# Optimization experiments

Measured on AMD Instinct MI355X. Metric: run time of the kernel, lower is better.

Reference implementation:

```python
import jax, jax.numpy as jnp
import numpy as np

TEMPERATURE = 0.07
EPS = 1e-12  # matches torch F.normalize eps
B, D = 16384, 128


def setup_inputs() -> dict:
    key = jax.random.key(0)
    k1, k2 = jax.random.split(key)
    anchor = jax.random.normal(k1, (B, D), dtype=jnp.float32)
    positive = jax.random.normal(k2, (B, D), dtype=jnp.float32)
    return {"anchor": anchor, "positive": positive}


def _l2_normalize(x):
    # torch F.normalize: x / max(||x||, eps)
    n = jnp.sqrt(jnp.sum(x * x, axis=-1, keepdims=True))
    return x / jnp.maximum(n, EPS)


def reference(anchor, positive):
    a = _l2_normalize(anchor)          # [B, D]
    p = _l2_normalize(positive)        # [B, D]
    pos_sim = jnp.sum(a * p, axis=-1) / TEMPERATURE            # [B]
    sim = jnp.matmul(a, p.T) / TEMPERATURE                     # [B, B]
    neg_inf = jnp.finfo(sim.dtype).min
    bsz = sim.shape[0]
    eye = jnp.eye(bsz, dtype=bool)
    neg_sim = jnp.where(eye, neg_inf, sim)                     # diag masked
    logits = jnp.concatenate([pos_sim[:, None], neg_sim], axis=1)  # [B, B+1]
    # cross-entropy with label 0: -log_softmax(logits)[:, 0]
    lse = jax.nn.logsumexp(logits, axis=1)
    loss = lse - logits[:, 0]
    return jnp.mean(loss)
```

## Files before the change

kernel.cpp:

```cpp
#include <hip/hip_runtime.h>
#include <stdint.h>

#define NROWS 16384
#define DIM 128

typedef __attribute__((ext_vector_type(8))) __bf16 bf16x8;
typedef __attribute__((ext_vector_type(4))) float f32x4;
typedef __attribute__((ext_vector_type(4))) unsigned int u32x4;

constexpr float TEMP_INV = 1.0f / 0.07f;
constexpr float LOG2E = 1.4426950408889634f;
constexpr float LN2 = 0.69314718055994531f;
constexpr float KAPPA = LOG2E * TEMP_INV;
constexpr float SQRT_KAPPA = 4.53981600f;

__device__ __forceinline__ ushort f2bf(float x) {
  uint32_t u = __builtin_bit_cast(uint32_t, x);
  uint32_t r = (u + 0x7fffu + ((u >> 16) & 1u)) >> 16;
  return (ushort)r;
}

__global__ __launch_bounds__(256) void prep_kernel(
    const float* __restrict__ anchor, const float* __restrict__ positive,
    ushort* __restrict__ abar, ushort* __restrict__ pbar,
    float* __restrict__ pos_u)
{
  const int tid = threadIdx.x;
  const int row = blockIdx.x * 16 + (tid >> 4);
  const int c0 = (tid & 15) * 8;

  const float4* a4 = reinterpret_cast<const float4*>(anchor + (size_t)row * DIM + c0);
  const float4* p4 = reinterpret_cast<const float4*>(positive + (size_t)row * DIM + c0);
  float4 a0 = a4[0], a1 = a4[1];
  float4 p0 = p4[0], p1 = p4[1];

  float af[8] = {a0.x, a0.y, a0.z, a0.w, a1.x, a1.y, a1.z, a1.w};
  float pf[8] = {p0.x, p0.y, p0.z, p0.w, p1.x, p1.y, p1.z, p1.w};

  float sa = 0.f, sp = 0.f, dp = 0.f;
#pragma unroll
  for (int j = 0; j < 8; ++j) {
    sa += af[j] * af[j];
    sp += pf[j] * pf[j];
    dp += af[j] * pf[j];
  }
#pragma unroll
  for (int m = 1; m <= 8; m <<= 1) {
    sa += __shfl_xor(sa, m, 64);
    sp += __shfl_xor(sp, m, 64);
    dp += __shfl_xor(dp, m, 64);
  }
  float inva = 1.0f / fmaxf(sqrtf(sa), 1e-12f);
  float invp = 1.0f / fmaxf(sqrtf(sp), 1e-12f);
  float ca = inva * SQRT_KAPPA;
  float cp = invp * SQRT_KAPPA;

  ushort ua[8], up[8];
#pragma unroll
  for (int j = 0; j < 8; ++j) {
    ua[j] = f2bf(af[j] * ca);
    up[j] = f2bf(pf[j] * cp);
  }
  *reinterpret_cast<uint4*>(abar + (size_t)row * DIM + c0) = *reinterpret_cast<uint4*>(ua);
  *reinterpret_cast<uint4*>(pbar + (size_t)row * DIM + c0) = *reinterpret_cast<uint4*>(up);

  if ((tid & 15) == 0)
    pos_u[row] = dp * inva * invp * KAPPA;
}

#define NSPLIT 8
#define BM 512
#define CPB (NROWS / NSPLIT)
#define BN 32
#define NIT (CPB / BN)

__global__ __launch_bounds__(512, 2) void lse_kernel(
    const ushort* __restrict__ abar,
    const ushort* __restrict__ pbar,
    float* __restrict__ sbuf )
{
  __shared__ alignas(16) char lds[2][BN * 256];

  const int tid = threadIdx.x;
  const int l = tid & 63;
  const int w = tid >> 6;
  const int r15 = l & 15;
  const int hi = l >> 4;

  const int bid = blockIdx.x;
  const int csplit = bid & 7;
  const int rowblk = bid >> 3;
  const int row0 = rowblk * BM + w * 64;
  const int col0 = csplit * CPB;

  const char* abase = (const char*)abar;
  const char* pbase = (const char*)pbar;

  bf16x8 afrag[4][4];
#pragma unroll
  for (int rg = 0; rg < 4; ++rg)
#pragma unroll
    for (int kk = 0; kk < 4; ++kk) {
      size_t off = (size_t)(row0 + rg * 16 + r15) * 256 + (size_t)(kk * 32 + hi * 8) * 2;
      u32x4 v = *reinterpret_cast<const u32x4*>(abase + off);
      afrag[rg][kk] = __builtin_bit_cast(bf16x8, v);
    }

  float s[4][4];
#pragma unroll
  for (int rg = 0; rg < 4; ++rg)
#pragma unroll
    for (int rr = 0; rr < 4; ++rr) s[rg][rr] = 0.f;

  const int strow = tid >> 4;
  const int stlds = strow * 256 + (((tid & 15) * 16) ^ ((strow & 7) << 4));

  u32x4 stg = *reinterpret_cast<const u32x4*>(pbase + (size_t)col0 * 256 + tid * 16);
  *reinterpret_cast<u32x4*>(&lds[0][stlds]) = stg;
  __syncthreads();

  for (int it = 0; it < NIT; ++it) {
    const int cur = it & 1;
    if (it + 1 < NIT)
      stg = *reinterpret_cast<const u32x4*>(
          pbase + (size_t)(col0 + (it + 1) * BN) * 256 + tid * 16);

#pragma unroll
    for (int ct = 0; ct < 2; ++ct) {
      const int tr = ct * 16 + r15;
      const int sw = (tr & 7) << 4;
      const char* base = &lds[cur][tr * 256];
      bf16x8 bfrag[4];
#pragma unroll
      for (int kk = 0; kk < 4; ++kk) {
        const int cb = kk * 64 + hi * 16;
        u32x4 v = *reinterpret_cast<const u32x4*>(base + (cb ^ sw));
        bfrag[kk] = __builtin_bit_cast(bf16x8, v);
      }
#pragma unroll
      for (int rg = 0; rg < 4; ++rg) {
        f32x4 acc = {0.f, 0.f, 0.f, 0.f};
#pragma unroll
        for (int kk = 0; kk < 4; ++kk)
          acc = __builtin_amdgcn_mfma_f32_16x16x32_bf16(afrag[rg][kk], bfrag[kk], acc, 0, 0, 0);
        s[rg][0] += __builtin_amdgcn_exp2f(acc[0]);
        s[rg][1] += __builtin_amdgcn_exp2f(acc[1]);
        s[rg][2] += __builtin_amdgcn_exp2f(acc[2]);
        s[rg][3] += __builtin_amdgcn_exp2f(acc[3]);
      }
    }
    __syncthreads();
    if (it + 1 < NIT) {
      *reinterpret_cast<u32x4*>(&lds[cur ^ 1][stlds]) = stg;
      __syncthreads();
    }
  }

#pragma unroll
  for (int rg = 0; rg < 4; ++rg)
#pragma unroll
    for (int rr = 0; rr < 4; ++rr) {
      float v = s[rg][rr];
      v += __shfl_xor(v, 1, 64);
      v += __shfl_xor(v, 2, 64);
      v += __shfl_xor(v, 4, 64);
      v += __shfl_xor(v, 8, 64);
      if (r15 == 0) {
        int grow = row0 + rg * 16 + hi * 4 + rr;
        sbuf[(size_t)csplit * NROWS + grow] = v;
      }
    }
}

__global__ __launch_bounds__(512) void finalize_kernel(
    const float* __restrict__ sbuf, const float* __restrict__ pos_u,
    float* __restrict__ out)
{
  const int tid = threadIdx.x;
  float acc = 0.f;
  for (int r = tid; r < NROWS; r += 512) {
    float s = 0.f;
#pragma unroll
    for (int c = 0; c < NSPLIT; ++c) s += sbuf[(size_t)c * NROWS + r];
    acc += LN2 * (__builtin_amdgcn_logf(s) - pos_u[r]);
  }
#pragma unroll
  for (int m = 1; m <= 32; m <<= 1) acc += __shfl_xor(acc, m, 64);
  __shared__ float red[8];
  if ((tid & 63) == 0) red[tid >> 6] = acc;
  __syncthreads();
  if (tid < 8) {
    float v = red[tid];
    v += __shfl_xor(v, 1, 64);
    v += __shfl_xor(v, 2, 64);
    v += __shfl_xor(v, 4, 64);
    if (tid == 0) out[0] = v * (1.0f / (float)NROWS);
  }
}

extern "C" void kernel_launch(void* const* d_in, const int* in_sizes, int n_in,
                              void* d_out, int out_size, void* d_ws, size_t ws_size,
                              hipStream_t stream) {
  const float* anchor = (const float*)d_in[0];
  const float* positive = (const float*)d_in[1];
  char* ws = (char*)d_ws;

  ushort* abar = (ushort*)ws;
  ushort* pbar = (ushort*)(ws + (size_t)NROWS * DIM * 2);
  float* pos_u = (float*)(ws + (size_t)NROWS * DIM * 4);
  float* sbuf = (float*)(ws + (size_t)NROWS * DIM * 4 + (size_t)NROWS * 4);
  float* out = (float*)d_out;

  prep_kernel<<<NROWS / 16, 256, 0, stream>>>(anchor, positive, abar, pbar, pos_u);
  lse_kernel<<<NSPLIT * (NROWS / BM), 512, 0, stream>>>(abar, pbar, sbuf);
  finalize_kernel<<<1, 512, 0, stream>>>(sbuf, pos_u, out);
}
```

Before: 92.73 us.

## Use direct global-to-LDS async loads with 4-deep buffering and smaller row tiles

Replaces the register-staged double buffer for positive tiles with global_load_lds direct copies into a 4-slot LDS ring, prefetching two tiles ahead and using vmcnt waits plus a single barrier per iteration. Halves rows per block (BM 512→256) to raise occupancy to 4 blocks per CU, adds setprio around the MFMA/exp section, and splits the single-block finalize into a parallel per-block partial reduction plus a tiny second pass. The aim is to hide load latency and remove the extra sync, at the cost of halving the reuse of each loaded B tile, so each block does less compute per load.

```diff
diff --git a/kernel.cpp b/kernel.cpp
--- a/kernel.cpp
+++ b/kernel.cpp
@@ -20,6 +20,12 @@
   return (ushort)r;
 }
 
+__device__ __forceinline__ void gload_lds16(const void* g, void* l) {
+  __builtin_amdgcn_global_load_lds(
+      (const __attribute__((address_space(1))) unsigned int*)g,
+      (__attribute__((address_space(3))) unsigned int*)l, 16, 0, 0);
+}
+
 __global__ __launch_bounds__(256) void prep_kernel(
     const float* __restrict__ anchor, const float* __restrict__ positive,
     ushort* __restrict__ abar, ushort* __restrict__ pbar,
@@ -69,17 +75,18 @@
 }
 
 #define NSPLIT 8
-#define BM 512
+#define BM 256
 #define CPB (NROWS / NSPLIT)
 #define BN 32
 #define NIT (CPB / BN)
-
-__global__ __launch_bounds__(512, 2) void lse_kernel(
+#define NBUF 4
+
+__global__ __launch_bounds__(512, 4) void lse_kernel(
     const ushort* __restrict__ abar,
     const ushort* __restrict__ pbar,
     float* __restrict__ sbuf )
 {
-  __shared__ alignas(16) char lds[2][BN * 256];
+  __shared__ alignas(16) char lds[NBUF][BN * 256];
 
   const int tid = threadIdx.x;
   const int l = tid & 63;
@@ -90,15 +97,15 @@
   const int bid = blockIdx.x;
   const int csplit = bid & 7;
   const int rowblk = bid >> 3;
-  const int row0 = rowblk * BM + w * 64;
+  const int row0 = rowblk * BM + w * 32;
   const int col0 = csplit * CPB;
 
   const char* abase = (const char*)abar;
   const char* pbase = (const char*)pbar;
 
-  bf16x8 afrag[4][4];
-#pragma unroll
-  for (int rg = 0; rg < 4; ++rg)
+  bf16x8 afrag[2][4];
+#pragma unroll
+  for (int rg = 0; rg < 2; ++rg)
 #pragma unroll
     for (int kk = 0; kk < 4; ++kk) {
       size_t off = (size_t)(row0 + rg * 16 + r15) * 256 + (size_t)(kk * 32 + hi * 8) * 2;
@@ -106,30 +113,42 @@
       afrag[rg][kk] = __builtin_bit_cast(bf16x8, v);
     }
 
-  float s[4][4];
-#pragma unroll
-  for (int rg = 0; rg < 4; ++rg)
+  float s[2][4];
+#pragma unroll
+  for (int rg = 0; rg < 2; ++rg)
 #pragma unroll
     for (int rr = 0; rr < 4; ++rr) s[rg][rr] = 0.f;
 
-  const int strow = tid >> 4;
-  const int stlds = strow * 256 + (((tid & 15) * 16) ^ ((strow & 7) << 4));
-
-  u32x4 stg = *reinterpret_cast<const u32x4*>(pbase + (size_t)col0 * 256 + tid * 16);
-  *reinterpret_cast<u32x4*>(&lds[0][stlds]) = stg;
-  __syncthreads();
+  const int trow = w * 4 + (l >> 4);
+  const size_t src0 = (size_t)(col0 + trow) * 256 + (size_t)(((l & 15) ^ (trow & 7)) * 16);
+  void* ldst[NBUF];
+#pragma unroll
+  for (int b = 0; b < NBUF; ++b) ldst[b] = &lds[b][w * 1024];
+
+  gload_lds16(pbase + src0, ldst[0]);
+  __builtin_amdgcn_sched_barrier(0);
+  gload_lds16(pbase + src0 + 8192, ldst[1]);
+  __builtin_amdgcn_sched_barrier(0);
 
   for (int it = 0; it < NIT; ++it) {
-    const int cur = it & 1;
-    if (it + 1 < NIT)
-      stg = *reinterpret_cast<const u32x4*>(
-          pbase + (size_t)(col0 + (it + 1) * BN) * 256 + tid * 16);
-
+    if (it < NIT - 1) {
+      asm volatile("s_waitcnt vmcnt(1)" ::: "memory");
+    } else {
+      asm volatile("s_waitcnt vmcnt(0)" ::: "memory");
+    }
+    __builtin_amdgcn_s_barrier();
+    asm volatile("" ::: "memory");
+    __builtin_amdgcn_sched_barrier(0);
+
+    if (it + 2 < NIT)
+      gload_lds16(pbase + src0 + (size_t)(it + 2) * 8192, ldst[(it + 2) & 3]);
+
+    const char* bufp = lds[it & 3];
 #pragma unroll
     for (int ct = 0; ct < 2; ++ct) {
       const int tr = ct * 16 + r15;
       const int sw = (tr & 7) << 4;
-      const char* base = &lds[cur][tr * 256];
+      const char* base = bufp + tr * 256;
       bf16x8 bfrag[4];
 #pragma unroll
       for (int kk = 0; kk < 4; ++kk) {
@@ -137,8 +156,9 @@
         u32x4 v = *reinterpret_cast<const u32x4*>(base + (cb ^ sw));
         bfrag[kk] = __builtin_bit_cast(bf16x8, v);
       }
-#pragma unroll
-      for (int rg = 0; rg < 4; ++rg) {
+      __builtin_amdgcn_s_setprio(1);
+#pragma unroll
+      for (int rg = 0; rg < 2; ++rg) {
         f32x4 acc = {0.f, 0.f, 0.f, 0.f};
 #pragma unroll
         for (int kk = 0; kk < 4; ++kk)
@@ -148,16 +168,12 @@
         s[rg][2] += __builtin_amdgcn_exp2f(acc[2]);
         s[rg][3] += __builtin_amdgcn_exp2f(acc[3]);
       }
-    }
-    __syncthreads();
-    if (it + 1 < NIT) {
-      *reinterpret_cast<u32x4*>(&lds[cur ^ 1][stlds]) = stg;
-      __syncthreads();
-    }
-  }
-
-#pragma unroll
-  for (int rg = 0; rg < 4; ++rg)
+      __builtin_amdgcn_s_setprio(0);
+    }
+  }
+
+#pragma unroll
+  for (int rg = 0; rg < 2; ++rg)
 #pragma unroll
     for (int rr = 0; rr < 4; ++rr) {
       float v = s[rg][rr];
@@ -172,30 +188,31 @@
     }
 }
 
-__global__ __launch_bounds__(512) void finalize_kernel(
+__global__ __launch_bounds__(256) void finalize1(
     const float* __restrict__ sbuf, const float* __restrict__ pos_u,
-    float* __restrict__ out)
+    float* __restrict__ partial)
 {
   const int tid = threadIdx.x;
-  float acc = 0.f;
-  for (int r = tid; r < NROWS; r += 512) {
-    float s = 0.f;
-#pragma unroll
-    for (int c = 0; c < NSPLIT; ++c) s += sbuf[(size_t)c * NROWS + r];
-    acc += LN2 * (__builtin_amdgcn_logf(s) - pos_u[r]);
-  }
+  const int r = blockIdx.x * 256 + tid;
+  float ssum = 0.f;
+#pragma unroll
+  for (int c = 0; c < NSPLIT; ++c) ssum += sbuf[(size_t)c * NROWS + r];
+  float acc = LN2 * (__builtin_amdgcn_logf(ssum) - pos_u[r]);
 #pragma unroll
   for (int m = 1; m <= 32; m <<= 1) acc += __shfl_xor(acc, m, 64);
-  __shared__ float red[8];
+  __shared__ float red[4];
   if ((tid & 63) == 0) red[tid >> 6] = acc;
   __syncthreads();
-  if (tid < 8) {
-    float v = red[tid];
-    v += __shfl_xor(v, 1, 64);
-    v += __shfl_xor(v, 2, 64);
-    v += __shfl_xor(v, 4, 64);
-    if (tid == 0) out[0] = v * (1.0f / (float)NROWS);
-  }
+  if (tid == 0) partial[blockIdx.x] = red[0] + red[1] + red[2] + red[3];
+}
+
+__global__ __launch_bounds__(64) void finalize2(
+    const float* __restrict__ partial, float* __restrict__ out)
+{
+  float v = partial[threadIdx.x];
+#pragma unroll
+  for (int m = 1; m <= 32; m <<= 1) v += __shfl_xor(v, m, 64);
+  if (threadIdx.x == 0) out[0] = v * (1.0f / (float)NROWS);
 }
 
 extern "C" void kernel_launch(void* const* d_in, const int* in_sizes, int n_in,
@@ -209,9 +226,12 @@
   ushort* pbar = (ushort*)(ws + (size_t)NROWS * DIM * 2);
   float* pos_u = (float*)(ws + (size_t)NROWS * DIM * 4);
   float* sbuf = (float*)(ws + (size_t)NROWS * DIM * 4 + (size_t)NROWS * 4);
+  float* partial = (float*)(ws + (size_t)NROWS * DIM * 4 + (size_t)NROWS * 4
+                            + (size_t)NSPLIT * NROWS * 4);
   float* out = (float*)d_out;
 
   prep_kernel<<<NROWS / 16, 256, 0, stream>>>(anchor, positive, abar, pbar, pos_u);
   lse_kernel<<<NSPLIT * (NROWS / BM), 512, 0, stream>>>(abar, pbar, sbuf);
-  finalize_kernel<<<1, 512, 0, stream>>>(sbuf, pos_u, out);
-}
+  finalize1<<<NROWS / 256, 256, 0, stream>>>(sbuf, pos_u, partial);
+  finalize2<<<1, 64, 0, stream>>>(partial, out);
+}
```

New measurement: 77.32 us. 1.2x faster.
